# Performance work log

Hardware: AMD Instinct MI355X
Metric: run time of the kernel (lower is better)

Reference implementation:

```python
import jax, jax.numpy as jnp
import numpy as np

B, C, H, W = 8, 64, 64, 64
IC = max(1, C // 8)  # inter_channels


def setup_inputs() -> dict:
    key = jax.random.key(0)
    ks = jax.random.split(key, 8)
    return {
        "x": jax.random.normal(ks[0], (B, C, H, W), dtype=jnp.float32),
        "theta_w": jax.random.normal(ks[1], (IC, C), dtype=jnp.float32) * 0.05,
        "theta_b": jnp.zeros((IC,), dtype=jnp.float32),
        "phi_w": jax.random.normal(ks[2], (IC, C), dtype=jnp.float32) * 0.05,
        "phi_b": jnp.zeros((IC,), dtype=jnp.float32),
        "g_w": jax.random.normal(ks[3], (C, C), dtype=jnp.float32) * 0.05,
        "g_b": jnp.zeros((C,), dtype=jnp.float32),
        "gamma": jax.random.normal(ks[4], (1,), dtype=jnp.float32),
    }


def reference(x, theta_w, theta_b, phi_w, phi_b, g_w, g_b, gamma):
    b, c, h, w = x.shape
    n = h * w
    xf = x.reshape(b, c, n)  # flatten spatial
    # 1x1 convs == per-pixel channel matmuls
    theta = jnp.einsum('ic,bcn->bin', theta_w, xf) + theta_b[None, :, None]  # [b, IC, n]
    phi = jnp.einsum('ic,bcn->bin', phi_w, xf) + phi_b[None, :, None]        # [b, IC, n]
    g = jnp.einsum('oc,bcn->bon', g_w, xf) + g_b[None, :, None]              # [b, C, n]
    # attn[b, q, k] = theta_q . phi_k, softmax over keys
    attn = jax.nn.softmax(jnp.einsum('biq,bik->bqk', theta, phi), axis=-1)   # [b, n, n]
    # out = g @ attn^T  (torch: bmm(g, attn.transpose(1,2)))
    out = jnp.einsum('bck,bqk->bcq', g, attn).reshape(b, c, h, w)
    return x + gamma[0] * out
```

## Files before the change

### kernel.cpp

```cpp
#include <hip/hip_runtime.h>
#include <cstddef>
#include <cstdint>


#define Bb 8
#define Cc 64
#define NN 4096
#define IC 8
#define VSTR 72
#define XSTR 72

typedef __attribute__((ext_vector_type(8)))  short bf16x8;
typedef __attribute__((ext_vector_type(16))) float f32x16;
typedef unsigned short ushort_t;
typedef unsigned int   uint_t;

#define LOG2E 1.4426950408889634f

static __device__ __forceinline__ uint_t f2bf(float x) {
    union { float f; uint_t u; } v; v.f = x;
    uint_t r = v.u + 0x7FFF + ((v.u >> 16) & 1);
    return r >> 16;
}
static __device__ __forceinline__ float bf2f(ushort_t u) {
    union { uint_t u; float f; } v; v.u = ((uint_t)u) << 16;
    return v.f;
}
static __device__ __forceinline__ float fexp2(float x) {
#if __has_builtin(__builtin_amdgcn_exp2f)
    return __builtin_amdgcn_exp2f(x);
#else
    return exp2f(x);
#endif
}
static __device__ __forceinline__ uint_t fbits(float x) {
    union { float f; uint_t u; } v; v.f = x; return v.u;
}
static __device__ __forceinline__ uint_t packbf(float e, float o) {
#if __has_builtin(__builtin_amdgcn_perm)
    return __builtin_amdgcn_perm(fbits(o), fbits(e), 0x07060302u);
#else
    return (fbits(e) >> 16) | (fbits(o) & 0xFFFF0000u);
#endif
}

union U4B { uint4 u; bf16x8 v; };

__global__ __launch_bounds__(256) void p1_kernel(
    const float* __restrict__ x,
    const float* __restrict__ theta_w, const float* __restrict__ theta_b,
    const float* __restrict__ phi_w,   const float* __restrict__ phi_b,
    const float* __restrict__ g_w,     const float* __restrict__ g_b,
    ushort_t* __restrict__ xbf, ushort_t* __restrict__ Wbf, float* __restrict__ biasf)
{
    const int t = threadIdx.x;
    const int bid = blockIdx.x;
    if (bid < 512) {
        __shared__ float Xt[64 * 68];
        const int b  = bid >> 6;
        const int nt = (bid & 63) * 64;
        const int c = t >> 2, nsg = t & 3;
        const float* xs = x + ((size_t)(b * 64 + c)) * NN + nt + nsg * 16;
        #pragma unroll
        for (int i = 0; i < 4; i++) {
            float4 v = ((const float4*)xs)[i];
            *(float4*)(Xt + c * 68 + nsg * 16 + i * 4) = v;
        }
        __syncthreads();
        const int n = t & 63, cs = t >> 6;
        uint_t wv[8];
        #pragma unroll
        for (int i = 0; i < 8; i++) {
            float e0 = Xt[(cs * 16 + 2 * i + 0) * 68 + n];
            float e1 = Xt[(cs * 16 + 2 * i + 1) * 68 + n];
            wv[i] = f2bf(e0) | (f2bf(e1) << 16);
        }
        ushort_t* dst = xbf + ((size_t)(b * NN + nt + n)) * 64 + cs * 16;
        *(uint4*)dst       = make_uint4(wv[0], wv[1], wv[2], wv[3]);
        *(uint4*)(dst + 8) = make_uint4(wv[4], wv[5], wv[6], wv[7]);
    } else {
        for (int i = t; i < 96 * 64; i += 256) {
            int row = i >> 6, c = i & 63;
            float v;
            if (row < 64)      v = g_w[row * 64 + c];
            else if (row < 72) v = theta_w[(row - 64) * 64 + c] * LOG2E;
            else if (row < 80) v = phi_w[(row - 72) * 64 + c];
            else               v = 0.0f;
            Wbf[i] = (ushort_t)f2bf(v);
        }
        if (t < 96) {
            float bv = (t < 64) ? g_b[t]
                     : (t < 72) ? theta_b[t - 64] * LOG2E
                     : (t < 80) ? phi_b[t - 72] : 0.0f;
            biasf[t] = bv;
        }
    }
}

__global__ __launch_bounds__(256) void p2_kernel(
    const ushort_t* __restrict__ xbf, const ushort_t* __restrict__ Wbf,
    const float* __restrict__ biasf,
    ushort_t* __restrict__ Qw, ushort_t* __restrict__ Kw, ushort_t* __restrict__ Vt)
{
    __shared__ ushort_t Xs[128 * XSTR];
    __shared__ float bs[96];

    const int t = threadIdx.x;
    const int lane = t & 63, w = t >> 6;
    const int l31 = lane & 31, hi = lane >> 5;
    const int b  = blockIdx.x >> 5;
    const int n0 = (blockIdx.x & 31) * 128;

    {
        const int n = t >> 1, h = t & 1;
        const ushort_t* src = xbf + ((size_t)(b * NN + n0 + n)) * 64 + h * 32;
        #pragma unroll
        for (int i = 0; i < 4; i++) {
            uint4 v = ((const uint4*)src)[i];
            *(uint4*)(Xs + n * XSTR + h * 32 + i * 8) = v;
        }
    }
    if (t < 96) bs[t] = biasf[t];
    __syncthreads();

    bf16x8 af[3][4];
    #pragma unroll
    for (int mt = 0; mt < 3; mt++)
        #pragma unroll
        for (int kc = 0; kc < 4; kc++)
            af[mt][kc] = *(const bf16x8*)(Wbf + (size_t)(mt * 32 + l31) * 64 + kc * 16 + hi * 8);

    f32x16 ac0 = {}, ac1 = {}, ac2 = {};
    #pragma unroll
    for (int kc = 0; kc < 4; kc++) {
        bf16x8 bv = *(const bf16x8*)(Xs + (w * 32 + l31) * XSTR + kc * 16 + hi * 8);
        ac0 = __builtin_amdgcn_mfma_f32_32x32x16_bf16(af[0][kc], bv, ac0, 0, 0, 0);
        ac1 = __builtin_amdgcn_mfma_f32_32x32x16_bf16(af[1][kc], bv, ac1, 0, 0, 0);
        ac2 = __builtin_amdgcn_mfma_f32_32x32x16_bf16(af[2][kc], bv, ac2, 0, 0, 0);
    }

    const int nw = n0 + w * 32;
    const int sig = ((l31 >> 3) & 1) * 16 + ((l31 >> 2) & 1) * 8 + ((l31 >> 4) & 1) * 4 + (l31 & 3);

    #pragma unroll
    for (int reg = 0; reg < 16; reg++) {
        int m = reg >> 2, r = reg & 3;
        {
            int ch = 4 * hi + 8 * m + r;
            float val = ac0[reg] + bs[ch];
            Vt[((size_t)(b * 64 + ch)) * NN + nw + sig] = (ushort_t)f2bf(val);
        }
        {
            int ch = 32 + 4 * hi + 8 * m + r;
            float val = ac1[reg] + bs[ch];
            Vt[((size_t)(b * 64 + ch)) * NN + nw + sig] = (ushort_t)f2bf(val);
        }
    }
    {
        float q0 = ac2[0] + bs[64 + 4 * hi + 0];
        float q1 = ac2[1] + bs[64 + 4 * hi + 1];
        float q2 = ac2[2] + bs[64 + 4 * hi + 2];
        float q3 = ac2[3] + bs[64 + 4 * hi + 3];
        uint2 qp = make_uint2(f2bf(q0) | (f2bf(q1) << 16), f2bf(q2) | (f2bf(q3) << 16));
        *(uint2*)(Qw + ((size_t)(b * NN) + nw + l31) * 8 + hi * 4) = qp;
        float p0 = ac2[4] + bs[72 + 4 * hi + 0];
        float p1 = ac2[5] + bs[72 + 4 * hi + 1];
        float p2 = ac2[6] + bs[72 + 4 * hi + 2];
        float p3 = ac2[7] + bs[72 + 4 * hi + 3];
        uint2 kp = make_uint2(f2bf(p0) | (f2bf(p1) << 16), f2bf(p2) | (f2bf(p3) << 16));
        *(uint2*)(Kw + ((size_t)(b * NN) + nw + l31) * 8 + hi * 4) = kp;
    }
}

#define COMPUTE_TILE(CURBUF, KC0, KC1)                                                    \
    {                                                                                     \
        __builtin_amdgcn_s_setprio(1);                                                    \
        U4B ka0_, ka1_; ka0_.u = KC0; ka1_.u = KC1;                                       \
        f32x16 S0 = __builtin_amdgcn_mfma_f32_32x32x16_bf16(ka0_.v, qf, zf, 0, 0, 0);     \
        f32x16 S1 = __builtin_amdgcn_mfma_f32_32x32x16_bf16(ka1_.v, qf, zf, 0, 0, 0);     \
        float p0[16], p1[16];                                                             \
        _Pragma("unroll") for (int i = 0; i < 16; i++) p0[i] = fexp2(S0[i]);              \
        _Pragma("unroll") for (int i = 0; i < 16; i++) p1[i] = fexp2(S1[i]);              \
        _Pragma("unroll") for (int i = 0; i < 16; i++) { lsum += p0[i]; lsum += p1[i]; }  \
        uint_t pk0[8], pk1[8];                                                            \
        _Pragma("unroll") for (int m = 0; m < 4; m++) {                                   \
            _Pragma("unroll") for (int rp = 0; rp < 2; rp++) {                            \
                pk0[m * 2 + rp] = packbf(p0[m * 4 + 2 * rp], p0[m * 4 + 2 * rp + 1]);     \
                pk1[m * 2 + rp] = packbf(p1[m * 4 + 2 * rp], p1[m * 4 + 2 * rp + 1]);     \
            }                                                                             \
        }                                                                                 \
        _Pragma("unroll") for (int kf = 0; kf < 2; kf++) {                                \
            _Pragma("unroll") for (int c = 0; c < 2; c++) {                               \
                U4B bu;                                                                   \
                if (kf == 0) bu.u = make_uint4(pk0[c * 2], pk0[c * 2 + 1],                \
                                               pk0[(c + 2) * 2], pk0[(c + 2) * 2 + 1]);  \
                else         bu.u = make_uint4(pk1[c * 2], pk1[c * 2 + 1],                \
                                               pk1[(c + 2) * 2], pk1[(c + 2) * 2 + 1]);  \
                bf16x8 av0 = *(const bf16x8*)(Vs[CURBUF] + (0 * 32 + l31) * VSTR + kf * 32 + c * 16 + hi * 8); \
                bf16x8 av1 = *(const bf16x8*)(Vs[CURBUF] + (1 * 32 + l31) * VSTR + kf * 32 + c * 16 + hi * 8); \
                acc0 = __builtin_amdgcn_mfma_f32_32x32x16_bf16(av0, bu.v, acc0, 0, 0, 0); \
                acc1 = __builtin_amdgcn_mfma_f32_32x32x16_bf16(av1, bu.v, acc1, 0, 0, 0); \
            }                                                                             \
        }                                                                                 \
        __builtin_amdgcn_s_setprio(0);                                                    \
    }

template <int FIN>
__global__ __launch_bounds__(512, 3) void attn_kernel(
    const ushort_t* __restrict__ Qw, const ushort_t* __restrict__ Kw,
    const ushort_t* __restrict__ Vt,
    ushort_t* __restrict__ P, float* __restrict__ L, int nsplit,
    const float* __restrict__ x, const float* __restrict__ gamma,
    float* __restrict__ out)
{
    __shared__ ushort_t Vs[2][64 * VSTR];

    const int t = threadIdx.x;
    const int lane = t & 63, w = t >> 6;
    const int l31 = lane & 31, hi = lane >> 5;

    int bid = blockIdx.x;
    const int b  = bid & 7;
    const int qt = (bid >> 3) & 15;
    const int s  = bid >> 7;
    const int q0 = qt * 256 + w * 32;
    const int keys = NN / nsplit;
    const int k0 = s * keys;
    const int ntiles = keys / 64;

    const ushort_t* Kb = Kw + (size_t)b * NN * 8;
    const ushort_t* Vb = Vt + (size_t)b * 64 * NN;

    bf16x8 qf = {};
    if (hi == 0)
        qf = *(const bf16x8*)(Qw + ((size_t)b * NN + q0 + l31) * 8);

    const int vch = t >> 3, vsg = t & 7;
    const ushort_t* vsrc = Vb + (size_t)vch * NN + k0 + vsg * 8;
    const int ws = vch * VSTR + vsg * 8;

    uint4 vA, vB;
    uint4 kA0, kA1, kB0 = {}, kB1 = {};

    vA = *(const uint4*)(vsrc);
    kA0 = *(const uint4*)(Kb + (size_t)(k0 + l31) * 8);
    kA1 = *(const uint4*)(Kb + (size_t)(k0 + 32 + l31) * 8);
    *(uint4*)(Vs[0] + ws) = vA;
    __syncthreads();
    vB = *(const uint4*)(vsrc + 64);
    kB0 = *(const uint4*)(Kb + (size_t)(k0 + 64 + l31) * 8);
    kB1 = *(const uint4*)(Kb + (size_t)(k0 + 64 + 32 + l31) * 8);

    f32x16 acc0 = {}, acc1 = {};
    float lsum = 0.0f;
    const f32x16 zf = {};

    for (int j = 0; j < ntiles; j += 2) {
        *(uint4*)(Vs[1] + ws) = vB;
        {
            const int jn = (j + 2 < ntiles) ? j + 2 : j;
            vA = *(const uint4*)(vsrc + (size_t)jn * 64);
        }
        COMPUTE_TILE(0, kA0, kA1)
        {
            const int jn = (j + 2 < ntiles) ? j + 2 : j;
            kA0 = *(const uint4*)(Kb + (size_t)(k0 + jn * 64 + l31) * 8);
            kA1 = *(const uint4*)(Kb + (size_t)(k0 + jn * 64 + 32 + l31) * 8);
        }
        asm volatile("s_waitcnt lgkmcnt(0)" ::: "memory");
        __builtin_amdgcn_s_barrier();
        asm volatile("" ::: "memory");

        *(uint4*)(Vs[0] + ws) = vA;
        {
            const int jn = (j + 3 < ntiles) ? j + 3 : j + 1;
            vB = *(const uint4*)(vsrc + (size_t)jn * 64);
        }
        COMPUTE_TILE(1, kB0, kB1)
        {
            const int jn = (j + 3 < ntiles) ? j + 3 : j + 1;
            kB0 = *(const uint4*)(Kb + (size_t)(k0 + jn * 64 + l31) * 8);
            kB1 = *(const uint4*)(Kb + (size_t)(k0 + jn * 64 + 32 + l31) * 8);
        }
        asm volatile("s_waitcnt lgkmcnt(0)" ::: "memory");
        __builtin_amdgcn_s_barrier();
        asm volatile("" ::: "memory");
    }

    float ltot = lsum + __shfl_xor(lsum, 32);

    if (!FIN) {
        ushort_t* Pb = P + ((size_t)(s * Bb + b) * 64) * NN;
        #pragma unroll
        for (int reg = 0; reg < 16; reg++) {
            int m = reg >> 2, r = reg & 3;
            int ch0 = 4 * hi + 8 * m + r;
            Pb[(size_t)ch0 * NN + q0 + l31]        = (ushort_t)f2bf(acc0[reg]);
            Pb[(size_t)(ch0 + 32) * NN + q0 + l31] = (ushort_t)f2bf(acc1[reg]);
        }
        if (lane < 32)
            L[(size_t)(s * Bb + b) * NN + q0 + lane] = ltot;
    } else {
        const float gm = gamma[0];
        const float inv = 1.0f / ltot;
        #pragma unroll
        for (int reg = 0; reg < 16; reg++) {
            int m = reg >> 2, r = reg & 3;
            int ch0 = 4 * hi + 8 * m + r;
            size_t i0 = ((size_t)(b * 64 + ch0)) * NN + q0 + l31;
            size_t i1 = ((size_t)(b * 64 + ch0 + 32)) * NN + q0 + l31;
            out[i0] = x[i0] + gm * acc0[reg] * inv;
            out[i1] = x[i1] + gm * acc1[reg] * inv;
        }
    }
}

__global__ __launch_bounds__(256) void combine_kernel(
    const ushort_t* __restrict__ P, const float* __restrict__ L,
    const float* __restrict__ x, const float* __restrict__ gamma,
    float* __restrict__ out, int nsplit)
{
    const int T = blockIdx.x * 256 + threadIdx.x;
    const int q = T & (NN - 1);
    const int r2 = T >> 12;
    const int b = r2 & 7;
    const int cg = r2 >> 3;

    float ls = 0.0f;
    for (int s = 0; s < nsplit; s++)
        ls += L[(size_t)(s * Bb + b) * NN + q];

    float a[16];
    #pragma unroll
    for (int j = 0; j < 16; j++) a[j] = 0.0f;
    for (int s = 0; s < nsplit; s++) {
        const ushort_t* Pb = P + ((size_t)(s * Bb + b) * 64 + cg * 16) * NN + q;
        #pragma unroll
        for (int j = 0; j < 16; j++)
            a[j] += bf2f(Pb[(size_t)j * NN]);
    }

    const float inv = 1.0f / ls;
    const float gm = gamma[0];
    #pragma unroll
    for (int j = 0; j < 16; j++) {
        size_t idx = ((size_t)(b * 64 + cg * 16 + j)) * NN + q;
        out[idx] = x[idx] + gm * a[j] * inv;
    }
}

extern "C" void kernel_launch(void* const* d_in, const int* in_sizes, int n_in,
                              void* d_out, int out_size, void* d_ws, size_t ws_size,
                              hipStream_t stream)
{
    const float* x       = (const float*)d_in[0];
    const float* theta_w = (const float*)d_in[1];
    const float* theta_b = (const float*)d_in[2];
    const float* phi_w   = (const float*)d_in[3];
    const float* phi_b   = (const float*)d_in[4];
    const float* g_w     = (const float*)d_in[5];
    const float* g_b     = (const float*)d_in[6];
    const float* gamma   = (const float*)d_in[7];
    float* out = (float*)d_out;

    char* p = (char*)d_ws;
    ushort_t* Qw  = (ushort_t*)p;  p += (size_t)Bb * NN * 8 * 2;
    ushort_t* Kw  = (ushort_t*)p;  p += (size_t)Bb * NN * 8 * 2;
    ushort_t* Vt  = (ushort_t*)p;  p += (size_t)Bb * 64 * NN * 2;
    ushort_t* xbf = (ushort_t*)p;  p += (size_t)Bb * NN * 64 * 2;
    ushort_t* Wbf = (ushort_t*)p;  p += 96 * 64 * 2;
    float*    biasf = (float*)p;   p += 96 * 4 + 128;
    char*     pbase = p;
    const size_t base_bytes  = (size_t)(pbase - (char*)d_ws);
    const size_t split_bytes = (size_t)Bb * 64 * NN * 2 + (size_t)Bb * NN * 4;

    int ns = 1;
    const int cands[3] = {4, 2, 1};
    for (int i = 0; i < 3; i++)
        if (base_bytes + (size_t)cands[i] * split_bytes <= ws_size) { ns = cands[i]; break; }

    ushort_t* P = (ushort_t*)pbase;
    float*    L = (float*)(pbase + (size_t)ns * Bb * 64 * NN * 2);

    p1_kernel<<<513, 256, 0, stream>>>(x, theta_w, theta_b, phi_w, phi_b, g_w, g_b,
                                       xbf, Wbf, biasf);
    p2_kernel<<<Bb * 32, 256, 0, stream>>>(xbf, Wbf, biasf, Qw, Kw, Vt);

    if (ns > 1) {
        attn_kernel<0><<<ns * Bb * 16, 512, 0, stream>>>(Qw, Kw, Vt, P, L, ns,
                                                         nullptr, nullptr, nullptr);
        combine_kernel<<<(Bb * NN * 4) / 256, 256, 0, stream>>>(P, L, x, gamma, out, ns);
    } else {
        attn_kernel<1><<<Bb * 16, 512, 0, stream>>>(Qw, Kw, Vt, P, L, 1,
                                                    x, gamma, out);
    }
}
```

Measured before the change: 53.41 us.

## Fuse bf16 conversion and weight packing into projection kernel, raise attn occupancy

Removes the separate p1 kernel that converted x to a bf16 pixel-major buffer and packed weights. p2 now loads fp32 x directly, transposes and converts through shared memory, and builds the bf16 weight matrix per block in LDS. This drops one launch and the xbf round trip through global memory, at the cost of redundant weight conversion in every block and more LDS per block. It also raises attn_kernel's launch_bounds min-blocks from 3 to 4, which may force register spills.

```diff
diff --git a/kernel.cpp b/kernel.cpp
--- a/kernel.cpp
+++ b/kernel.cpp
@@ -46,64 +46,17 @@
 
 union U4B { uint4 u; bf16x8 v; };
 
-__global__ __launch_bounds__(256) void p1_kernel(
+__global__ __launch_bounds__(256) void p2_kernel(
     const float* __restrict__ x,
     const float* __restrict__ theta_w, const float* __restrict__ theta_b,
     const float* __restrict__ phi_w,   const float* __restrict__ phi_b,
     const float* __restrict__ g_w,     const float* __restrict__ g_b,
-    ushort_t* __restrict__ xbf, ushort_t* __restrict__ Wbf, float* __restrict__ biasf)
-{
-    const int t = threadIdx.x;
-    const int bid = blockIdx.x;
-    if (bid < 512) {
-        __shared__ float Xt[64 * 68];
-        const int b  = bid >> 6;
-        const int nt = (bid & 63) * 64;
-        const int c = t >> 2, nsg = t & 3;
-        const float* xs = x + ((size_t)(b * 64 + c)) * NN + nt + nsg * 16;
-        #pragma unroll
-        for (int i = 0; i < 4; i++) {
-            float4 v = ((const float4*)xs)[i];
-            *(float4*)(Xt + c * 68 + nsg * 16 + i * 4) = v;
-        }
-        __syncthreads();
-        const int n = t & 63, cs = t >> 6;
-        uint_t wv[8];
-        #pragma unroll
-        for (int i = 0; i < 8; i++) {
-            float e0 = Xt[(cs * 16 + 2 * i + 0) * 68 + n];
-            float e1 = Xt[(cs * 16 + 2 * i + 1) * 68 + n];
-            wv[i] = f2bf(e0) | (f2bf(e1) << 16);
-        }
-        ushort_t* dst = xbf + ((size_t)(b * NN + nt + n)) * 64 + cs * 16;
-        *(uint4*)dst       = make_uint4(wv[0], wv[1], wv[2], wv[3]);
-        *(uint4*)(dst + 8) = make_uint4(wv[4], wv[5], wv[6], wv[7]);
-    } else {
-        for (int i = t; i < 96 * 64; i += 256) {
-            int row = i >> 6, c = i & 63;
-            float v;
-            if (row < 64)      v = g_w[row * 64 + c];
-            else if (row < 72) v = theta_w[(row - 64) * 64 + c] * LOG2E;
-            else if (row < 80) v = phi_w[(row - 72) * 64 + c];
-            else               v = 0.0f;
-            Wbf[i] = (ushort_t)f2bf(v);
-        }
-        if (t < 96) {
-            float bv = (t < 64) ? g_b[t]
-                     : (t < 72) ? theta_b[t - 64] * LOG2E
-                     : (t < 80) ? phi_b[t - 72] : 0.0f;
-            biasf[t] = bv;
-        }
-    }
-}
-
-__global__ __launch_bounds__(256) void p2_kernel(
-    const ushort_t* __restrict__ xbf, const ushort_t* __restrict__ Wbf,
-    const float* __restrict__ biasf,
     ushort_t* __restrict__ Qw, ushort_t* __restrict__ Kw, ushort_t* __restrict__ Vt)
 {
+    __shared__ float    Xt[64 * 132];
     __shared__ ushort_t Xs[128 * XSTR];
-    __shared__ float bs[96];
+    __shared__ ushort_t Wl[96 * 64];
+    __shared__ float    bs[96];
 
     const int t = threadIdx.x;
     const int lane = t & 63, w = t >> 6;
@@ -112,23 +65,52 @@
     const int n0 = (blockIdx.x & 31) * 128;
 
     {
-        const int n = t >> 1, h = t & 1;
-        const ushort_t* src = xbf + ((size_t)(b * NN + n0 + n)) * 64 + h * 32;
-        #pragma unroll
-        for (int i = 0; i < 4; i++) {
-            uint4 v = ((const uint4*)src)[i];
-            *(uint4*)(Xs + n * XSTR + h * 32 + i * 8) = v;
-        }
-    }
-    if (t < 96) bs[t] = biasf[t];
+        const int c = t >> 2, seg = t & 3;
+        const float* xs = x + ((size_t)(b * 64 + c)) * NN + n0 + seg * 32;
+        #pragma unroll
+        for (int i = 0; i < 8; i++) {
+            float4 v = ((const float4*)xs)[i];
+            *(float4*)(Xt + c * 132 + seg * 32 + i * 4) = v;
+        }
+    }
+    for (int i = t; i < 96 * 64; i += 256) {
+        int row = i >> 6, c = i & 63;
+        float v;
+        if (row < 64)      v = g_w[i];
+        else if (row < 72) v = theta_w[(row - 64) * 64 + c] * LOG2E;
+        else if (row < 80) v = phi_w[(row - 72) * 64 + c];
+        else               v = 0.0f;
+        Wl[i] = (ushort_t)f2bf(v);
+    }
+    if (t < 96) {
+        bs[t] = (t < 64) ? g_b[t]
+              : (t < 72) ? theta_b[t - 64] * LOG2E
+              : (t < 80) ? phi_b[t - 72] : 0.0f;
+    }
     __syncthreads();
 
+    {
+        const int n = t & 127, half = t >> 7;
+        uint_t wv[16];
+        #pragma unroll
+        for (int i = 0; i < 16; i++) {
+            float e0 = Xt[(half * 32 + 2 * i + 0) * 132 + n];
+            float e1 = Xt[(half * 32 + 2 * i + 1) * 132 + n];
+            wv[i] = f2bf(e0) | (f2bf(e1) << 16);
+        }
+        #pragma unroll
+        for (int i = 0; i < 4; i++)
+            *(uint4*)(Xs + n * XSTR + half * 32 + i * 8) =
+                make_uint4(wv[4 * i], wv[4 * i + 1], wv[4 * i + 2], wv[4 * i + 3]);
+    }
+    __syncthreads();
+
     bf16x8 af[3][4];
     #pragma unroll
     for (int mt = 0; mt < 3; mt++)
         #pragma unroll
         for (int kc = 0; kc < 4; kc++)
-            af[mt][kc] = *(const bf16x8*)(Wbf + (size_t)(mt * 32 + l31) * 64 + kc * 16 + hi * 8);
+            af[mt][kc] = *(const bf16x8*)(Wl + (size_t)(mt * 32 + l31) * 64 + kc * 16 + hi * 8);
 
     f32x16 ac0 = {}, ac1 = {}, ac2 = {};
     #pragma unroll
@@ -206,7 +188,7 @@
     }
 
 template <int FIN>
-__global__ __launch_bounds__(512, 3) void attn_kernel(
+__global__ __launch_bounds__(512, 4) void attn_kernel(
     const ushort_t* __restrict__ Qw, const ushort_t* __restrict__ Kw,
     const ushort_t* __restrict__ Vt,
     ushort_t* __restrict__ P, float* __restrict__ L, int nsplit,
@@ -367,9 +349,6 @@
     ushort_t* Qw  = (ushort_t*)p;  p += (size_t)Bb * NN * 8 * 2;
     ushort_t* Kw  = (ushort_t*)p;  p += (size_t)Bb * NN * 8 * 2;
     ushort_t* Vt  = (ushort_t*)p;  p += (size_t)Bb * 64 * NN * 2;
-    ushort_t* xbf = (ushort_t*)p;  p += (size_t)Bb * NN * 64 * 2;
-    ushort_t* Wbf = (ushort_t*)p;  p += 96 * 64 * 2;
-    float*    biasf = (float*)p;   p += 96 * 4 + 128;
     char*     pbase = p;
     const size_t base_bytes  = (size_t)(pbase - (char*)d_ws);
     const size_t split_bytes = (size_t)Bb * 64 * NN * 2 + (size_t)Bb * NN * 4;
@@ -382,9 +361,8 @@
     ushort_t* P = (ushort_t*)pbase;
     float*    L = (float*)(pbase + (size_t)ns * Bb * 64 * NN * 2);
 
-    p1_kernel<<<513, 256, 0, stream>>>(x, theta_w, theta_b, phi_w, phi_b, g_w, g_b,
-                                       xbf, Wbf, biasf);
-    p2_kernel<<<Bb * 32, 256, 0, stream>>>(xbf, Wbf, biasf, Qw, Kw, Vt);
+    p2_kernel<<<Bb * 32, 256, 0, stream>>>(x, theta_w, theta_b, phi_w, phi_b,
+                                           g_w, g_b, Qw, Kw, Vt);
 
     if (ns > 1) {
         attn_kernel<0><<<ns * Bb * 16, 512, 0, stream>>>(Qw, Kw, Vt, P, L, ns,
```

After: 51.76 us (median of 2 runs). 1.03x faster.
